# Optimization experiments

Measured on AMD Instinct MI355X. Metric: run time of the kernel, lower is better.

## Reference

```python
import jax, jax.numpy as jnp
import numpy as np

NUM_HEADS = 16
DIM_HEAD = 64
DIM = 1024
SCALE = DIM ** (-0.5)  # NOTE: source scales by model dim, not dim_head


def setup_inputs() -> dict:
    key = jax.random.key(0)
    ks = jax.random.split(key, 6)
    b, n, d = 2, 2048, DIM
    return {
        "x": jax.random.normal(ks[0], (b, n, d), dtype=jnp.float32),
        "mask": jnp.ones((b, n), dtype=bool),
        "Wq": jax.random.normal(ks[1], (NUM_HEADS * DIM_HEAD, d), dtype=jnp.float32) * 0.02,
        "Wk": jax.random.normal(ks[2], (DIM_HEAD, d), dtype=jnp.float32) * 0.02,
        "Wv": jax.random.normal(ks[3], (DIM_HEAD, d), dtype=jnp.float32) * 0.02,
        "Wfc": jax.random.normal(ks[4], (d, NUM_HEADS * DIM_HEAD), dtype=jnp.float32) * 0.02,
        "bfc": jnp.zeros((d,), dtype=jnp.float32),
    }


def reference(x, mask, Wq, Wk, Wv, Wfc, bfc):
    b, n, _ = x.shape
    # projections (nn.Linear: y = x @ W.T)
    q = (x @ Wq.T).reshape(b, n, NUM_HEADS, DIM_HEAD).transpose(0, 2, 1, 3)  # b h n d
    k = x @ Wk.T  # b n d  (single shared MQA head)
    v = x @ Wv.T  # b n d
    energy = jnp.einsum("bhid,bjd->bhij", q, k) * SCALE  # b h i j
    mask_value = -jnp.finfo(energy.dtype).max
    # input mask: k_mask is all ones in source, so only query rows are masked
    q_mask = mask[:, None, :, None]  # b 1 i 1
    energy = jnp.where(q_mask, energy, mask_value)
    # causal mask: positions j > i are masked (i == j since self-attention)
    i = jnp.arange(n)
    causal = i[:, None] < i[None, :]  # True where future
    energy = jnp.where(causal[None, None, :, :], mask_value, energy)
    attn = jax.nn.softmax(energy, axis=-1)
    # dropout_rate = 0.0 -> identity
    out = jnp.einsum("bhij,bjd->bhid", attn, v)
    out = out.transpose(0, 2, 1, 3).reshape(b, n, NUM_HEADS * DIM_HEAD)
    return out @ Wfc.T + bfc
```

## Files before the change

kernel.cpp:

```cpp
#include <hip/hip_runtime.h>
#include <math.h>

#define NH 16
#define DH 64
#define DM 1024
#define NS 2048
#define BB 2
#define MR (BB * NS)
#define LDQ 1152
#define C_EXP 0.0450842201f

typedef unsigned short u16;
typedef __attribute__((ext_vector_type(8))) short short8;
typedef __attribute__((ext_vector_type(4))) float floatx4;
typedef __attribute__((ext_vector_type(4))) u16 u16x4;

#if __has_builtin(__builtin_amdgcn_exp2f)
#define EXP2(x) __builtin_amdgcn_exp2f(x)
#else
#define EXP2(x) exp2f(x)
#endif

static __device__ __forceinline__ u16 f2bf(float f) {
  union { float f; unsigned u; } v; v.f = f;
  unsigned r = v.u + 0x7fffu + ((v.u >> 16) & 1u);
  return (u16)(r >> 16);
}
static __device__ __forceinline__ u16 f2bf_fast(float f) {
  union { float f; unsigned u; } v; v.f = f;
  return (u16)((v.u + 0x8000u) >> 16);
}

#define GLDS16(gp, lp)                                                        \
  __builtin_amdgcn_global_load_lds(                                           \
      (const __attribute__((address_space(1))) void*)(const void*)(gp),       \
      (__attribute__((address_space(3))) void*)(void*)(lp), 16, 0, 0)

__global__ __launch_bounds__(256) void cast_all(
    const float* __restrict__ x, const float* __restrict__ wq,
    const float* __restrict__ wk, const float* __restrict__ wv,
    const float* __restrict__ wfc, u16* __restrict__ xb,
    u16* __restrict__ wqkvb, u16* __restrict__ wfcb) {
  const int NX = MR * DM / 4, NQ = DM * DM / 4, NK = DH * DM / 4;
  int id = blockIdx.x * 256 + threadIdx.x;
  const float* src;
  u16* dst;
  int off;
  if (id < NX) { src = x; dst = xb; off = id; }
  else if (id < NX + NQ) { src = wq; dst = wqkvb; off = id - NX; }
  else if (id < NX + NQ + NK) { src = wk; dst = wqkvb + (size_t)DM * DM; off = id - NX - NQ; }
  else if (id < NX + NQ + 2 * NK) { src = wv; dst = wqkvb + (size_t)(DM + DH) * DM; off = id - NX - NQ - NK; }
  else { src = wfc; dst = wfcb; off = id - NX - NQ - 2 * NK; }
  float4 f = ((const float4*)src)[off];
  u16x4 o;
  o[0] = f2bf(f.x); o[1] = f2bf(f.y); o[2] = f2bf(f.z); o[3] = f2bf(f.w);
  ((u16x4*)dst)[off] = o;
}

__global__ __launch_bounds__(256) void gemm_bf16(
    const u16* __restrict__ A, const u16* __restrict__ W,
    const float* __restrict__ bias, void* __restrict__ Cout,
    int M, int N, int K, int ldc, int out_bf16) {
  __shared__ u16 As[2][128 * 32];
  __shared__ u16 Ws[2][128 * 32];
  const int tid = threadIdx.x;
  const int lane = tid & 63;
  const int lr = lane & 15, quad = lane >> 4;
  const int wave = tid >> 6, wr = wave >> 1, wc = wave & 1;
  const int m0 = blockIdx.y * 128, n0 = blockIdx.x * 128;

  const int ci0 = wave * 128 + lane, ci1 = ci0 + 64;
  const int r0 = ci0 >> 2, r1 = ci1 >> 2;
  const int cg0 = (ci0 & 3) ^ ((r0 >> 1) & 3);
  const int cg1 = (ci1 & 3) ^ ((r1 >> 1) & 3);
  const u16* gA0 = A + (size_t)(m0 + r0) * K + cg0 * 8;
  const u16* gA1 = A + (size_t)(m0 + r1) * K + cg1 * 8;
  const u16* gW0 = W + (size_t)(n0 + r0) * K + cg0 * 8;
  const u16* gW1 = W + (size_t)(n0 + r1) * K + cg1 * 8;
  const int lo0 = wave * 1024, lo1 = wave * 1024 + 512;

  floatx4 acc[4][4] = {};
  const int nt = K >> 5;

  GLDS16(gA0, &As[0][lo0]);
  GLDS16(gA1, &As[0][lo1]);
  GLDS16(gW0, &Ws[0][lo0]);
  GLDS16(gW1, &Ws[0][lo1]);

  for (int t = 0; t < nt; ++t) {
    __syncthreads();
    if (t + 1 < nt) {
      const int ko = (t + 1) << 5;
      const int nb = (t + 1) & 1;
      GLDS16(gA0 + ko, &As[nb][lo0]);
      GLDS16(gA1 + ko, &As[nb][lo1]);
      GLDS16(gW0 + ko, &Ws[nb][lo0]);
      GLDS16(gW1 + ko, &Ws[nb][lo1]);
    }
    const u16* as = As[t & 1];
    const u16* ws = Ws[t & 1];
    short8 af[4], wf[4];
#pragma unroll
    for (int mi = 0; mi < 4; ++mi) {
      int rr = wr * 64 + mi * 16 + lr;
      af[mi] = *(const short8*)&as[rr * 32 + ((quad ^ ((rr >> 1) & 3)) << 3)];
    }
#pragma unroll
    for (int nj = 0; nj < 4; ++nj) {
      int rc = wc * 64 + nj * 16 + lr;
      wf[nj] = *(const short8*)&ws[rc * 32 + ((quad ^ ((rc >> 1) & 3)) << 3)];
    }
#pragma unroll
    for (int mi = 0; mi < 4; ++mi)
#pragma unroll
      for (int nj = 0; nj < 4; ++nj)
        acc[mi][nj] = __builtin_amdgcn_mfma_f32_16x16x32_bf16(
            af[mi], wf[nj], acc[mi][nj], 0, 0, 0);
  }

#pragma unroll
  for (int mi = 0; mi < 4; ++mi) {
#pragma unroll
    for (int nj = 0; nj < 4; ++nj) {
      int col = n0 + wc * 64 + nj * 16 + lr;
      float badd = bias ? bias[col] : 0.f;
#pragma unroll
      for (int r = 0; r < 4; ++r) {
        int row = m0 + wr * 64 + mi * 16 + quad * 4 + r;
        float v = acc[mi][nj][r] + badd;
        if (out_bf16)
          ((u16*)Cout)[(size_t)row * ldc + col] = f2bf(v);
        else
          ((float*)Cout)[(size_t)row * ldc + col] = v;
      }
    }
  }
}

__global__ __launch_bounds__(128) void attn_mfma(
    const u16* __restrict__ qkv,
    u16* __restrict__ aob) {
  __shared__ u16 Ks[2][64 * 64];
  __shared__ u16 Vt[2][64 * 72];
  __shared__ u16 Ps[2][16 * 72];

  const int b = blockIdx.z;
  const int p = blockIdx.x;
  const int head = blockIdx.y;
  const int tid = threadIdx.x;
  const int lane = tid & 63;
  const int lr = lane & 15, quad = lane >> 4;
  const int w = tid >> 6;
  const size_t rowb = (size_t)b * NS;
  const u16* kvK = qkv + rowb * LDQ + 1024;
  const u16* kvV = qkv + rowb * LDQ + 1088;

  int kr[4], kc[4];
#pragma unroll
  for (int g = 0; g < 4; ++g) {
    int ci = w * 256 + g * 64 + lane;
    kr[g] = ci >> 3;
    kc[g] = (ci & 7) ^ (kr[g] & 7);
  }

  const int dg = tid & 15;
  const int jc = tid >> 4;

  for (int phase = 0; phase < 2; ++phase) {
    const int s = (phase == 0) ? (63 - p) : p;
    const int i0q = s * 32;
    const int ntp = (s >> 1) + 1;
    const int irow = i0q + w * 16 + quad * 4;

    const u16* qp = qkv + (rowb + i0q + w * 16 + lr) * LDQ + head * DH;
    short8 aq0 = *(const short8*)(qp + quad * 8);
    short8 aq1 = *(const short8*)(qp + 32 + quad * 8);

    floatx4 o[4] = {};
    float lacc[4] = {0.f, 0.f, 0.f, 0.f};
    u16x4 vr[8];

#pragma unroll
    for (int g = 0; g < 4; ++g)
      GLDS16(kvK + (size_t)kr[g] * LDQ + kc[g] * 8, &Ks[0][(w * 256 + g * 64) * 8]);
#pragma unroll
    for (int jj = 0; jj < 8; ++jj)
      vr[jj] = *(const u16x4*)(kvV + (size_t)(jc * 8 + jj) * LDQ + dg * 4);

    for (int t = 0; t < ntp; ++t) {
      const int buf = t & 1;
#pragma unroll
      for (int dd = 0; dd < 4; ++dd) {
        short8 col;
#pragma unroll
        for (int jj = 0; jj < 8; ++jj) col[jj] = (short)vr[jj][dd];
        *(short8*)&Vt[buf][(dg * 4 + dd) * 72 + (((jc + dg) & 7) << 3)] = col;
      }
      __syncthreads();

      if (t + 1 < ntp) {
        const int j0n = (t + 1) * 64;
        const int nb2 = buf ^ 1;
#pragma unroll
        for (int g = 0; g < 4; ++g)
          GLDS16(kvK + (size_t)(j0n + kr[g]) * LDQ + kc[g] * 8,
                 &Ks[nb2][(w * 256 + g * 64) * 8]);
#pragma unroll
        for (int jj = 0; jj < 8; ++jj)
          vr[jj] = *(const u16x4*)(kvV + (size_t)(j0n + jc * 8 + jj) * LDQ + dg * 4);
      }

      const int j0 = t * 64;
      const u16* ksb = Ks[buf];
      const u16* vtb = Vt[buf];
      floatx4 sv[4];
#pragma unroll
      for (int jb = 0; jb < 4; ++jb) {
        const int krow = jb * 16 + lr;
        short8 bk0 = *(const short8*)&ksb[krow * 64 + ((quad ^ (krow & 7)) << 3)];
        short8 bk1 = *(const short8*)&ksb[krow * 64 + (((4 + quad) ^ (krow & 7)) << 3)];
        floatx4 z = {};
        z = __builtin_amdgcn_mfma_f32_16x16x32_bf16(aq0, bk0, z, 0, 0, 0);
        z = __builtin_amdgcn_mfma_f32_16x16x32_bf16(aq1, bk1, z, 0, 0, 0);
        sv[jb] = z;
      }

      u16* Pw = Ps[w];
      const bool lastt = (t == ntp - 1);
#pragma unroll
      for (int jb = 0; jb < 4; ++jb) {
#pragma unroll
        for (int r = 0; r < 4; ++r) {
          float pe = EXP2(sv[jb][r] * C_EXP);
          if (lastt && (j0 + jb * 16 + lr > irow + r)) pe = 0.f;
          lacc[r] += pe;
          const int row = quad * 4 + r, colj = jb * 16 + lr;
          Pw[row * 72 + ((((colj >> 3) + (row >> 1)) & 7) << 3) + (colj & 7)] =
              f2bf_fast(pe);
        }
      }
      asm volatile("s_waitcnt lgkmcnt(0)" ::: "memory");
      short8 ap0 = *(const short8*)&Pw[lr * 72 + (((quad + (lr >> 1)) & 7) << 3)];
      short8 ap1 = *(const short8*)&Pw[lr * 72 + (((4 + quad + (lr >> 1)) & 7) << 3)];

#pragma unroll
      for (int nb = 0; nb < 4; ++nb) {
        const int d0 = nb * 16 + lr;
        short8 bv0 = *(const short8*)&vtb[d0 * 72 + (((quad + (d0 >> 2)) & 7) << 3)];
        short8 bv1 = *(const short8*)&vtb[d0 * 72 + (((4 + quad + (d0 >> 2)) & 7) << 3)];
        o[nb] = __builtin_amdgcn_mfma_f32_16x16x32_bf16(ap0, bv0, o[nb], 0, 0, 0);
        o[nb] = __builtin_amdgcn_mfma_f32_16x16x32_bf16(ap1, bv1, o[nb], 0, 0, 0);
      }
    }

#pragma unroll
    for (int r = 0; r < 4; ++r) {
      float l = lacc[r];
      l += __shfl_xor(l, 1);
      l += __shfl_xor(l, 2);
      l += __shfl_xor(l, 4);
      l += __shfl_xor(l, 8);
      lacc[r] = l;
    }
#pragma unroll
    for (int nb = 0; nb < 4; ++nb)
#pragma unroll
      for (int r = 0; r < 4; ++r)
        aob[(rowb + irow + r) * DM + head * DH + nb * 16 + lr] =
            f2bf(o[nb][r] / lacc[r]);

    __syncthreads();
  }
}

extern "C" void kernel_launch(void* const* d_in, const int* in_sizes, int n_in,
                              void* d_out, int out_size, void* d_ws, size_t ws_size,
                              hipStream_t stream) {
  const float* x = (const float*)d_in[0];
  const float* Wq = (const float*)d_in[2];
  const float* Wk = (const float*)d_in[3];
  const float* Wv = (const float*)d_in[4];
  const float* Wfc = (const float*)d_in[5];
  const float* bfc = (const float*)d_in[6];

  u16* xb = (u16*)d_ws;
  u16* wqkvb = xb + (size_t)MR * DM;
  u16* wfcb = wqkvb + (size_t)LDQ * DM;
  u16* qkv = wfcb + (size_t)DM * DM;
  u16* aob = xb;

  dim3 blk(256);
  cast_all<<<dim3((MR * DM + DM * DM * 2 + DH * DM * 2) / 1024), blk, 0, stream>>>(
      x, Wq, Wk, Wv, Wfc, xb, wqkvb, wfcb);
  gemm_bf16<<<dim3(LDQ / 128, MR / 128), blk, 0, stream>>>(
      xb, wqkvb, nullptr, qkv, MR, LDQ, DM, LDQ, 1);
  attn_mfma<<<dim3(32, NH, BB), dim3(128), 0, stream>>>(qkv, aob);
  gemm_bf16<<<dim3(DM / 128, MR / 128), blk, 0, stream>>>(
      aob, wfcb, bfc, d_out, MR, DM, DM, DM, 0);
}
```

Before: 187.5 us.

## Emit transposed V from QKV GEMM and shrink GEMM to single-wave 64x64 tiles

The QKV GEMM now writes the V block (column tile 17) transposed into a separate buffer, so the attention kernel can stream V^T tiles straight into LDS with async global-to-LDS loads. This removes the per-tile register transpose and the padded LDS stores in the attention inner loop. The GEMM is also reworked into one-wave 64x64 tiles with no barrier, relying on vmcnt waits, which gives more blocks but less data reuse per block. The transposed V store uses strided scattered writes and needs extra workspace.

```diff
diff --git a/kernel.cpp b/kernel.cpp
--- a/kernel.cpp
+++ b/kernel.cpp
@@ -57,57 +57,59 @@
   ((u16x4*)dst)[off] = o;
 }
 
-__global__ __launch_bounds__(256) void gemm_bf16(
+__global__ __launch_bounds__(64) void gemm_bf16(
     const u16* __restrict__ A, const u16* __restrict__ W,
     const float* __restrict__ bias, void* __restrict__ Cout,
-    int M, int N, int K, int ldc, int out_bf16) {
-  __shared__ u16 As[2][128 * 32];
-  __shared__ u16 Ws[2][128 * 32];
-  const int tid = threadIdx.x;
-  const int lane = tid & 63;
+    u16* __restrict__ vT, int M, int N, int K, int ldc, int out_bf16,
+    int v_bx) {
+  __shared__ u16 As[2][64 * 32];
+  __shared__ u16 Ws[2][64 * 32];
+  const int lane = threadIdx.x;
   const int lr = lane & 15, quad = lane >> 4;
-  const int wave = tid >> 6, wr = wave >> 1, wc = wave & 1;
-  const int m0 = blockIdx.y * 128, n0 = blockIdx.x * 128;
-
-  const int ci0 = wave * 128 + lane, ci1 = ci0 + 64;
-  const int r0 = ci0 >> 2, r1 = ci1 >> 2;
-  const int cg0 = (ci0 & 3) ^ ((r0 >> 1) & 3);
-  const int cg1 = (ci1 & 3) ^ ((r1 >> 1) & 3);
-  const u16* gA0 = A + (size_t)(m0 + r0) * K + cg0 * 8;
-  const u16* gA1 = A + (size_t)(m0 + r1) * K + cg1 * 8;
-  const u16* gW0 = W + (size_t)(n0 + r0) * K + cg0 * 8;
-  const u16* gW1 = W + (size_t)(n0 + r1) * K + cg1 * 8;
-  const int lo0 = wave * 1024, lo1 = wave * 1024 + 512;
+  const int m0 = blockIdx.y * 64, n0 = blockIdx.x * 64;
+
+  const u16* gA[4];
+  const u16* gW[4];
+#pragma unroll
+  for (int g = 0; g < 4; ++g) {
+    int ci = g * 64 + lane;
+    int row = ci >> 2;
+    int cg = (ci & 3) ^ ((row >> 1) & 3);
+    gA[g] = A + (size_t)(m0 + row) * K + cg * 8;
+    gW[g] = W + (size_t)(n0 + row) * K + cg * 8;
+  }
 
   floatx4 acc[4][4] = {};
   const int nt = K >> 5;
 
-  GLDS16(gA0, &As[0][lo0]);
-  GLDS16(gA1, &As[0][lo1]);
-  GLDS16(gW0, &Ws[0][lo0]);
-  GLDS16(gW1, &Ws[0][lo1]);
+#pragma unroll
+  for (int g = 0; g < 4; ++g) GLDS16(gA[g], &As[0][g * 512]);
+#pragma unroll
+  for (int g = 0; g < 4; ++g) GLDS16(gW[g], &Ws[0][g * 512]);
 
   for (int t = 0; t < nt; ++t) {
-    __syncthreads();
     if (t + 1 < nt) {
       const int ko = (t + 1) << 5;
       const int nb = (t + 1) & 1;
-      GLDS16(gA0 + ko, &As[nb][lo0]);
-      GLDS16(gA1 + ko, &As[nb][lo1]);
-      GLDS16(gW0 + ko, &Ws[nb][lo0]);
-      GLDS16(gW1 + ko, &Ws[nb][lo1]);
+#pragma unroll
+      for (int g = 0; g < 4; ++g) GLDS16(gA[g] + ko, &As[nb][g * 512]);
+#pragma unroll
+      for (int g = 0; g < 4; ++g) GLDS16(gW[g] + ko, &Ws[nb][g * 512]);
+      asm volatile("s_waitcnt vmcnt(8)" ::: "memory");
+    } else {
+      asm volatile("s_waitcnt vmcnt(0)" ::: "memory");
     }
     const u16* as = As[t & 1];
     const u16* ws = Ws[t & 1];
     short8 af[4], wf[4];
 #pragma unroll
     for (int mi = 0; mi < 4; ++mi) {
-      int rr = wr * 64 + mi * 16 + lr;
+      int rr = mi * 16 + lr;
       af[mi] = *(const short8*)&as[rr * 32 + ((quad ^ ((rr >> 1) & 3)) << 3)];
     }
 #pragma unroll
     for (int nj = 0; nj < 4; ++nj) {
-      int rc = wc * 64 + nj * 16 + lr;
+      int rc = nj * 16 + lr;
       wf[nj] = *(const short8*)&ws[rc * 32 + ((quad ^ ((rc >> 1) & 3)) << 3)];
     }
 #pragma unroll
@@ -118,15 +120,27 @@
             af[mi], wf[nj], acc[mi][nj], 0, 0, 0);
   }
 
+  if (vT && blockIdx.x == v_bx) {
+#pragma unroll
+    for (int mi = 0; mi < 4; ++mi)
+#pragma unroll
+      for (int nj = 0; nj < 4; ++nj)
+#pragma unroll
+        for (int r = 0; r < 4; ++r)
+          vT[(size_t)(nj * 16 + lr) * MR + m0 + mi * 16 + quad * 4 + r] =
+              f2bf(acc[mi][nj][r]);
+    return;
+  }
+
 #pragma unroll
   for (int mi = 0; mi < 4; ++mi) {
 #pragma unroll
     for (int nj = 0; nj < 4; ++nj) {
-      int col = n0 + wc * 64 + nj * 16 + lr;
+      int col = n0 + nj * 16 + lr;
       float badd = bias ? bias[col] : 0.f;
 #pragma unroll
       for (int r = 0; r < 4; ++r) {
-        int row = m0 + wr * 64 + mi * 16 + quad * 4 + r;
+        int row = m0 + mi * 16 + quad * 4 + r;
         float v = acc[mi][nj][r] + badd;
         if (out_bf16)
           ((u16*)Cout)[(size_t)row * ldc + col] = f2bf(v);
@@ -139,9 +153,10 @@
 
 __global__ __launch_bounds__(128) void attn_mfma(
     const u16* __restrict__ qkv,
+    const u16* __restrict__ vT,
     u16* __restrict__ aob) {
   __shared__ u16 Ks[2][64 * 64];
-  __shared__ u16 Vt[2][64 * 72];
+  __shared__ u16 Vt[2][64 * 64];
   __shared__ u16 Ps[2][16 * 72];
 
   const int b = blockIdx.z;
@@ -153,18 +168,15 @@
   const int w = tid >> 6;
   const size_t rowb = (size_t)b * NS;
   const u16* kvK = qkv + rowb * LDQ + 1024;
-  const u16* kvV = qkv + rowb * LDQ + 1088;
-
-  int kr[4], kc[4];
+  const u16* vTb = vT + rowb;
+
+  int srow[4], scg[4];
 #pragma unroll
   for (int g = 0; g < 4; ++g) {
     int ci = w * 256 + g * 64 + lane;
-    kr[g] = ci >> 3;
-    kc[g] = (ci & 7) ^ (kr[g] & 7);
-  }
-
-  const int dg = tid & 15;
-  const int jc = tid >> 4;
+    srow[g] = ci >> 3;
+    scg[g] = (ci & 7) ^ (srow[g] & 7);
+  }
 
   for (int phase = 0; phase < 2; ++phase) {
     const int s = (phase == 0) ? (63 - p) : p;
@@ -178,24 +190,18 @@
 
     floatx4 o[4] = {};
     float lacc[4] = {0.f, 0.f, 0.f, 0.f};
-    u16x4 vr[8];
 
 #pragma unroll
     for (int g = 0; g < 4; ++g)
-      GLDS16(kvK + (size_t)kr[g] * LDQ + kc[g] * 8, &Ks[0][(w * 256 + g * 64) * 8]);
-#pragma unroll
-    for (int jj = 0; jj < 8; ++jj)
-      vr[jj] = *(const u16x4*)(kvV + (size_t)(jc * 8 + jj) * LDQ + dg * 4);
+      GLDS16(kvK + (size_t)srow[g] * LDQ + scg[g] * 8,
+             &Ks[0][(w * 256 + g * 64) * 8]);
+#pragma unroll
+    for (int g = 0; g < 4; ++g)
+      GLDS16(vTb + (size_t)srow[g] * MR + scg[g] * 8,
+             &Vt[0][(w * 256 + g * 64) * 8]);
 
     for (int t = 0; t < ntp; ++t) {
       const int buf = t & 1;
-#pragma unroll
-      for (int dd = 0; dd < 4; ++dd) {
-        short8 col;
-#pragma unroll
-        for (int jj = 0; jj < 8; ++jj) col[jj] = (short)vr[jj][dd];
-        *(short8*)&Vt[buf][(dg * 4 + dd) * 72 + (((jc + dg) & 7) << 3)] = col;
-      }
       __syncthreads();
 
       if (t + 1 < ntp) {
@@ -203,11 +209,12 @@
         const int nb2 = buf ^ 1;
 #pragma unroll
         for (int g = 0; g < 4; ++g)
-          GLDS16(kvK + (size_t)(j0n + kr[g]) * LDQ + kc[g] * 8,
+          GLDS16(kvK + (size_t)(j0n + srow[g]) * LDQ + scg[g] * 8,
                  &Ks[nb2][(w * 256 + g * 64) * 8]);
 #pragma unroll
-        for (int jj = 0; jj < 8; ++jj)
-          vr[jj] = *(const u16x4*)(kvV + (size_t)(j0n + jc * 8 + jj) * LDQ + dg * 4);
+        for (int g = 0; g < 4; ++g)
+          GLDS16(vTb + (size_t)srow[g] * MR + j0n + scg[g] * 8,
+                 &Vt[nb2][(w * 256 + g * 64) * 8]);
       }
 
       const int j0 = t * 64;
@@ -246,8 +253,8 @@
 #pragma unroll
       for (int nb = 0; nb < 4; ++nb) {
         const int d0 = nb * 16 + lr;
-        short8 bv0 = *(const short8*)&vtb[d0 * 72 + (((quad + (d0 >> 2)) & 7) << 3)];
-        short8 bv1 = *(const short8*)&vtb[d0 * 72 + (((4 + quad + (d0 >> 2)) & 7) << 3)];
+        short8 bv0 = *(const short8*)&vtb[d0 * 64 + ((quad ^ (d0 & 7)) << 3)];
+        short8 bv1 = *(const short8*)&vtb[d0 * 64 + (((4 + quad) ^ (d0 & 7)) << 3)];
         o[nb] = __builtin_amdgcn_mfma_f32_16x16x32_bf16(ap0, bv0, o[nb], 0, 0, 0);
         o[nb] = __builtin_amdgcn_mfma_f32_16x16x32_bf16(ap1, bv1, o[nb], 0, 0, 0);
       }
@@ -287,14 +294,14 @@
   u16* wqkvb = xb + (size_t)MR * DM;
   u16* wfcb = wqkvb + (size_t)LDQ * DM;
   u16* qkv = wfcb + (size_t)DM * DM;
+  u16* vT = qkv + (size_t)MR * LDQ;
   u16* aob = xb;
 
-  dim3 blk(256);
-  cast_all<<<dim3((MR * DM + DM * DM * 2 + DH * DM * 2) / 1024), blk, 0, stream>>>(
-      x, Wq, Wk, Wv, Wfc, xb, wqkvb, wfcb);
-  gemm_bf16<<<dim3(LDQ / 128, MR / 128), blk, 0, stream>>>(
-      xb, wqkvb, nullptr, qkv, MR, LDQ, DM, LDQ, 1);
-  attn_mfma<<<dim3(32, NH, BB), dim3(128), 0, stream>>>(qkv, aob);
-  gemm_bf16<<<dim3(DM / 128, MR / 128), blk, 0, stream>>>(
-      aob, wfcb, bfc, d_out, MR, DM, DM, DM, 0);
-}
+  cast_all<<<dim3((MR * DM + DM * DM * 2 + DH * DM * 2) / 1024), dim3(256), 0,
+             stream>>>(x, Wq, Wk, Wv, Wfc, xb, wqkvb, wfcb);
+  gemm_bf16<<<dim3(LDQ / 64, MR / 64), dim3(64), 0, stream>>>(
+      xb, wqkvb, nullptr, qkv, vT, MR, LDQ, DM, LDQ, 1, 17);
+  attn_mfma<<<dim3(32, NH, BB), dim3(128), 0, stream>>>(qkv, vT, aob);
+  gemm_bf16<<<dim3(DM / 64, MR / 64), dim3(64), 0, stream>>>(
+      aob, wfcb, bfc, d_out, nullptr, MR, DM, DM, DM, 0, -1);
+}
```

Result: no change. 185.8 us (-0.9%).

## Emit transposed V from QKV GEMM epilogue and async-load it in attention

Applied to the files above, without the earlier changes.

The QKV projection GEMM now writes the V columns transposed (d-major) into a separate buffer from the block stripe that holds them. The attention kernel then loads V tiles straight into LDS with the same async global-to-LDS path used for K, dropping the register transpose and the padded V layout. The GEMM grid is also reordered so M varies fastest across block x. Trade-offs: the transposed epilogue store for that stripe is strided and uncoalesced, and the kernel needs extra workspace for vT.

```diff
diff --git a/kernel.cpp b/kernel.cpp
--- a/kernel.cpp
+++ b/kernel.cpp
@@ -60,14 +60,15 @@
 __global__ __launch_bounds__(256) void gemm_bf16(
     const u16* __restrict__ A, const u16* __restrict__ W,
     const float* __restrict__ bias, void* __restrict__ Cout,
-    int M, int N, int K, int ldc, int out_bf16) {
+    u16* __restrict__ vT, int M, int N, int K, int ldc, int out_bf16,
+    int v_by) {
   __shared__ u16 As[2][128 * 32];
   __shared__ u16 Ws[2][128 * 32];
   const int tid = threadIdx.x;
   const int lane = tid & 63;
   const int lr = lane & 15, quad = lane >> 4;
   const int wave = tid >> 6, wr = wave >> 1, wc = wave & 1;
-  const int m0 = blockIdx.y * 128, n0 = blockIdx.x * 128;
+  const int m0 = blockIdx.x * 128, n0 = blockIdx.y * 128;
 
   const int ci0 = wave * 128 + lane, ci1 = ci0 + 64;
   const int r0 = ci0 >> 2, r1 = ci1 >> 2;
@@ -118,6 +119,7 @@
             af[mi], wf[nj], acc[mi][nj], 0, 0, 0);
   }
 
+  const bool vstripe = (v_by >= 0) && ((int)blockIdx.y == v_by);
 #pragma unroll
   for (int mi = 0; mi < 4; ++mi) {
 #pragma unroll
@@ -128,7 +130,9 @@
       for (int r = 0; r < 4; ++r) {
         int row = m0 + wr * 64 + mi * 16 + quad * 4 + r;
         float v = acc[mi][nj][r] + badd;
-        if (out_bf16)
+        if (vstripe && col >= 1088)
+          vT[(size_t)(col - 1088) * MR + row] = f2bf(v);
+        else if (out_bf16)
           ((u16*)Cout)[(size_t)row * ldc + col] = f2bf(v);
         else
           ((float*)Cout)[(size_t)row * ldc + col] = v;
@@ -139,9 +143,10 @@
 
 __global__ __launch_bounds__(128) void attn_mfma(
     const u16* __restrict__ qkv,
+    const u16* __restrict__ vT,
     u16* __restrict__ aob) {
   __shared__ u16 Ks[2][64 * 64];
-  __shared__ u16 Vt[2][64 * 72];
+  __shared__ u16 Vt[2][64 * 64];
   __shared__ u16 Ps[2][16 * 72];
 
   const int b = blockIdx.z;
@@ -153,18 +158,15 @@
   const int w = tid >> 6;
   const size_t rowb = (size_t)b * NS;
   const u16* kvK = qkv + rowb * LDQ + 1024;
-  const u16* kvV = qkv + rowb * LDQ + 1088;
-
-  int kr[4], kc[4];
+  const u16* vTb = vT + rowb;
+
+  int srow[4], scg[4];
 #pragma unroll
   for (int g = 0; g < 4; ++g) {
     int ci = w * 256 + g * 64 + lane;
-    kr[g] = ci >> 3;
-    kc[g] = (ci & 7) ^ (kr[g] & 7);
-  }
-
-  const int dg = tid & 15;
-  const int jc = tid >> 4;
+    srow[g] = ci >> 3;
+    scg[g] = (ci & 7) ^ (srow[g] & 7);
+  }
 
   for (int phase = 0; phase < 2; ++phase) {
     const int s = (phase == 0) ? (63 - p) : p;
@@ -178,24 +180,18 @@
 
     floatx4 o[4] = {};
     float lacc[4] = {0.f, 0.f, 0.f, 0.f};
-    u16x4 vr[8];
 
 #pragma unroll
     for (int g = 0; g < 4; ++g)
-      GLDS16(kvK + (size_t)kr[g] * LDQ + kc[g] * 8, &Ks[0][(w * 256 + g * 64) * 8]);
-#pragma unroll
-    for (int jj = 0; jj < 8; ++jj)
-      vr[jj] = *(const u16x4*)(kvV + (size_t)(jc * 8 + jj) * LDQ + dg * 4);
+      GLDS16(kvK + (size_t)srow[g] * LDQ + scg[g] * 8,
+             &Ks[0][(w * 256 + g * 64) * 8]);
+#pragma unroll
+    for (int g = 0; g < 4; ++g)
+      GLDS16(vTb + (size_t)srow[g] * MR + scg[g] * 8,
+             &Vt[0][(w * 256 + g * 64) * 8]);
 
     for (int t = 0; t < ntp; ++t) {
       const int buf = t & 1;
-#pragma unroll
-      for (int dd = 0; dd < 4; ++dd) {
-        short8 col;
-#pragma unroll
-        for (int jj = 0; jj < 8; ++jj) col[jj] = (short)vr[jj][dd];
-        *(short8*)&Vt[buf][(dg * 4 + dd) * 72 + (((jc + dg) & 7) << 3)] = col;
-      }
       __syncthreads();
 
       if (t + 1 < ntp) {
@@ -203,11 +199,12 @@
         const int nb2 = buf ^ 1;
 #pragma unroll
         for (int g = 0; g < 4; ++g)
-          GLDS16(kvK + (size_t)(j0n + kr[g]) * LDQ + kc[g] * 8,
+          GLDS16(kvK + (size_t)(j0n + srow[g]) * LDQ + scg[g] * 8,
                  &Ks[nb2][(w * 256 + g * 64) * 8]);
 #pragma unroll
-        for (int jj = 0; jj < 8; ++jj)
-          vr[jj] = *(const u16x4*)(kvV + (size_t)(j0n + jc * 8 + jj) * LDQ + dg * 4);
+        for (int g = 0; g < 4; ++g)
+          GLDS16(vTb + (size_t)srow[g] * MR + j0n + scg[g] * 8,
+                 &Vt[nb2][(w * 256 + g * 64) * 8]);
       }
 
       const int j0 = t * 64;
@@ -246,8 +243,8 @@
 #pragma unroll
       for (int nb = 0; nb < 4; ++nb) {
         const int d0 = nb * 16 + lr;
-        short8 bv0 = *(const short8*)&vtb[d0 * 72 + (((quad + (d0 >> 2)) & 7) << 3)];
-        short8 bv1 = *(const short8*)&vtb[d0 * 72 + (((4 + quad + (d0 >> 2)) & 7) << 3)];
+        short8 bv0 = *(const short8*)&vtb[d0 * 64 + ((quad ^ (d0 & 7)) << 3)];
+        short8 bv1 = *(const short8*)&vtb[d0 * 64 + (((4 + quad) ^ (d0 & 7)) << 3)];
         o[nb] = __builtin_amdgcn_mfma_f32_16x16x32_bf16(ap0, bv0, o[nb], 0, 0, 0);
         o[nb] = __builtin_amdgcn_mfma_f32_16x16x32_bf16(ap1, bv1, o[nb], 0, 0, 0);
       }
@@ -287,14 +284,14 @@
   u16* wqkvb = xb + (size_t)MR * DM;
   u16* wfcb = wqkvb + (size_t)LDQ * DM;
   u16* qkv = wfcb + (size_t)DM * DM;
+  u16* vT = qkv + (size_t)MR * LDQ;
   u16* aob = xb;
 
-  dim3 blk(256);
-  cast_all<<<dim3((MR * DM + DM * DM * 2 + DH * DM * 2) / 1024), blk, 0, stream>>>(
-      x, Wq, Wk, Wv, Wfc, xb, wqkvb, wfcb);
-  gemm_bf16<<<dim3(LDQ / 128, MR / 128), blk, 0, stream>>>(
-      xb, wqkvb, nullptr, qkv, MR, LDQ, DM, LDQ, 1);
-  attn_mfma<<<dim3(32, NH, BB), dim3(128), 0, stream>>>(qkv, aob);
-  gemm_bf16<<<dim3(DM / 128, MR / 128), blk, 0, stream>>>(
-      aob, wfcb, bfc, d_out, MR, DM, DM, DM, 0);
-}
+  cast_all<<<dim3((MR * DM + DM * DM * 2 + DH * DM * 2) / 1024), dim3(256), 0,
+             stream>>>(x, Wq, Wk, Wv, Wfc, xb, wqkvb, wfcb);
+  gemm_bf16<<<dim3(MR / 128, LDQ / 128), dim3(256), 0, stream>>>(
+      xb, wqkvb, nullptr, qkv, vT, MR, LDQ, DM, LDQ, 1, 8);
+  attn_mfma<<<dim3(32, NH, BB), dim3(128), 0, stream>>>(qkv, vT, aob);
+  gemm_bf16<<<dim3(MR / 128, DM / 128), dim3(256), 0, stream>>>(
+      aob, wfcb, bfc, d_out, nullptr, MR, DM, DM, DM, 0, -1);
+}
```

Measured after the change: 185.6 us. No clear change (-1.1%).
